# Kernel tuning notes

Measured on AMD Instinct MI355X. Metric: run time of the kernel, lower is better.

Reference implementation:

```python
import jax, jax.numpy as jnp
import numpy as np

HEAD_SIZE = 64


def setup_inputs() -> dict:
    key = jax.random.key(0)
    ks = jax.random.split(key, 10)
    B, S, D, H, hs = 4, 2048, 768, 12, HEAD_SIZE
    F = 4 * D
    sd = lambda n: 1.0 / np.sqrt(n)
    return {
        "x": jax.random.normal(ks[0], (B, S, D), jnp.float32),
        "Wq": jax.random.normal(ks[1], (H, D, hs), jnp.float32) * sd(D),
        "Wk": jax.random.normal(ks[2], (H, D, hs), jnp.float32) * sd(D),
        "Wv": jax.random.normal(ks[3], (H, D, hs), jnp.float32) * sd(D),
        "Wo": jax.random.normal(ks[4], (D, D), jnp.float32) * sd(D),
        "bo": jnp.zeros((D,), jnp.float32),
        "W1": jax.random.normal(ks[5], (D, F), jnp.float32) * sd(D),
        "b1": jnp.zeros((F,), jnp.float32),
        "W2": jax.random.normal(ks[6], (F, D), jnp.float32) * sd(F),
        "b2": jnp.zeros((D,), jnp.float32),
    }


def reference(x, Wq, Wk, Wv, Wo, bo, W1, b1, W2, b2):
    B, S, D = x.shape
    hs = Wq.shape[-1]
    # per-head projections (no bias), vectorized over heads: [B,H,S,hs]
    q = jnp.einsum("bsd,hde->bhse", x, Wq)
    k = jnp.einsum("bsd,hde->bhse", x, Wk)
    v = jnp.einsum("bsd,hde->bhse", x, Wv)
    # causal attention scores [B,H,S,S], scaled by sqrt(head_size)
    scores = jnp.einsum("bhse,bhte->bhst", q, k) / jnp.sqrt(jnp.float32(hs))
    causal = jnp.tril(jnp.ones((S, S), dtype=bool))
    scores = jnp.where(causal, scores, -jnp.inf)
    attn = jax.nn.softmax(scores, axis=-1)
    z = jnp.einsum("bhst,bhte->bhse", attn, v)
    # concat heads along feature dim (head order preserved) -> [B,S,D]
    z = z.transpose(0, 2, 1, 3).reshape(B, S, D)
    # output projection + residual
    z = z @ Wo + bo + x
    # FFN + residual
    h = jax.nn.relu(z @ W1 + b1)
    return h @ W2 + b2 + z
```

## Files before the change

### kernel.cpp

```cpp
#include <hip/hip_runtime.h>


typedef __attribute__((ext_vector_type(4))) float f32x4;
typedef __attribute__((ext_vector_type(8))) short bf16x8;
typedef __attribute__((ext_vector_type(4))) unsigned short u16x4;

#define GLB_AS __attribute__((address_space(1)))
#define LDS_AS __attribute__((address_space(3)))

__device__ __forceinline__ unsigned short f2bf(float f) {
  unsigned int u = __float_as_uint(f);
  u = (u + 0x7FFFu + ((u >> 16) & 1u)) >> 16;
  return (unsigned short)u;
}

__device__ __forceinline__ void gload16(const void* g, void* l) {
  __builtin_amdgcn_global_load_lds((const GLB_AS unsigned int*)g,
                                   (LDS_AS unsigned int*)l, 16, 0, 0);
}

__device__ __forceinline__ int xcd_swz(int orig, int nwg) {
  int q = nwg >> 3, r = nwg & 7;
  int xcd = orig & 7, rest = orig >> 3;
  return (xcd < r ? xcd * (q + 1) : r * (q + 1) + (xcd - r) * q) + rest;
}

#define VMW4 asm volatile("s_waitcnt vmcnt(4)" ::: "memory")
#define VMW0 asm volatile("s_waitcnt vmcnt(0)" ::: "memory")

__global__ void castx(const float* __restrict__ in, unsigned short* __restrict__ out, int n) {
  int i = (blockIdx.x * 256 + threadIdx.x) * 4;
  if (i < n) {
    float4 f = *(const float4*)&in[i];
    u16x4 o;
    o[0] = f2bf(f.x); o[1] = f2bf(f.y); o[2] = f2bf(f.z); o[3] = f2bf(f.w);
    *(u16x4*)&out[i] = o;
  }
}

__global__ void tcast(const float* __restrict__ in, unsigned short* __restrict__ out,
                      int R, int C, float scale) {
  __shared__ float tile[32][33];
  const float* inb = in + (size_t)blockIdx.z * R * C;
  unsigned short* outb = out + (size_t)blockIdx.z * R * C;
  int bx = blockIdx.x * 32;
  int by = blockIdx.y * 32;
  int tx = threadIdx.x, ty = threadIdx.y;
  #pragma unroll
  for (int i = 0; i < 32; i += 8)
    tile[ty + i][tx] = inb[(size_t)(by + ty + i) * C + bx + tx];
  __syncthreads();
  #pragma unroll
  for (int i = 0; i < 32; i += 8)
    outb[(size_t)(bx + ty + i) * R + by + tx] = f2bf(tile[tx][ty + i] * scale);
}

__global__ void tcast3(const float* __restrict__ Wq, const float* __restrict__ Wk,
                       const float* __restrict__ Wv, unsigned short* __restrict__ out,
                       float qscale) {
  __shared__ float tile[32][33];
  const int R = 768, C = 64;
  int z = blockIdx.z, wsel = z / 12, head = z % 12;
  const float* in = (wsel == 0 ? Wq : wsel == 1 ? Wk : Wv) + (size_t)head * R * C;
  unsigned short* outb = out + (size_t)wsel * R * R + (size_t)head * R * C;
  float scale = wsel == 0 ? qscale : 1.0f;
  int bx = blockIdx.x * 32;
  int by = blockIdx.y * 32;
  int tx = threadIdx.x, ty = threadIdx.y;
  #pragma unroll
  for (int i = 0; i < 32; i += 8)
    tile[ty + i][tx] = in[(size_t)(by + ty + i) * C + bx + tx];
  __syncthreads();
  #pragma unroll
  for (int i = 0; i < 32; i += 8)
    outb[(size_t)(bx + ty + i) * R + by + tx] = f2bf(tile[tx][ty + i] * scale);
}

__global__ void vtrans(const unsigned short* __restrict__ v, unsigned short* __restrict__ vT) {
  __shared__ unsigned short tile[32][33];
  int bh = blockIdx.z, b = bh / 12, h = bh % 12;
  int s0 = blockIdx.x * 32, e0 = blockIdx.y * 32;
  int tx = threadIdx.x, ty = threadIdx.y;
  #pragma unroll
  for (int i = 0; i < 32; i += 8)
    tile[ty + i][tx] = v[(size_t)(b * 2048 + s0 + ty + i) * 768 + h * 64 + e0 + tx];
  __syncthreads();
  #pragma unroll
  for (int i = 0; i < 32; i += 8)
    vT[(size_t)((b * 12 + h) * 64 + e0 + ty + i) * 2048 + s0 + tx] = tile[tx][ty + i];
}

template <int EPI, int MAP>
__global__ void gemm_bf16(const unsigned short* __restrict__ A,
                          const unsigned short* __restrict__ Bt,
                          const float* __restrict__ bias,
                          const float* __restrict__ resid,
                          float* __restrict__ Cf,
                          unsigned short* __restrict__ Cb,
                          int M, int N, int K, int gy, size_t segN) {
  __shared__ unsigned short Alds[2][128 * 32];
  __shared__ unsigned short Blds[2][128 * 32];
  const int tid = threadIdx.x;
  const int lane = tid & 63;
  const int w = tid >> 6;
  const int wm = w & 1, wn = w >> 1;

  int bm, bn;
  if constexpr (MAP == 1) {
    const int xcd = blockIdx.x & 7, rest = blockIdx.x >> 3;
    const int bnper = gy >> 3;
    bm = (rest / bnper) * 128;
    bn = (xcd * bnper + rest % bnper) * 128;
  } else if constexpr (MAP == 2) {
    const int xcd = blockIdx.x & 7, rest = blockIdx.x >> 3;
    if (rest < 128) { bm = (rest >> 1) * 128; bn = (xcd * 2 + (rest & 1)) * 128; }
    else { int r2 = rest - 128; bm = (xcd * 8 + (r2 & 7)) * 128; bn = (16 + (r2 >> 3)) * 128; }
  } else {
    const int wg = xcd_swz(blockIdx.x, gridDim.x);
    const int gsz = 8 * gy;
    const int group = wg / gsz;
    const int rem = wg - group * gsz;
    bm = (group * 8 + (rem & 7)) * 128;
    bn = (rem >> 3) * 128;
  }

  f32x4 acc[4][4] = {};

  const int r0 = tid >> 2;
  const int c0 = (tid & 3) * 8;

  #pragma unroll
  for (int i = 0; i < 2; ++i) {
    int row = r0 + i * 64;
    gload16(&A[(size_t)(bm + row) * K + c0], &Alds[0][row * 32 + c0]);
    gload16(&Bt[(size_t)(bn + row) * K + c0], &Blds[0][row * 32 + c0]);
  }
  __syncthreads();

  int buf = 0;
  for (int k0 = 0; k0 < K; k0 += 32) {
    if (k0 + 32 < K) {
      #pragma unroll
      for (int i = 0; i < 2; ++i) {
        int row = r0 + i * 64;
        gload16(&A[(size_t)(bm + row) * K + k0 + 32 + c0], &Alds[buf ^ 1][row * 32 + c0]);
        gload16(&Bt[(size_t)(bn + row) * K + k0 + 32 + c0], &Blds[buf ^ 1][row * 32 + c0]);
      }
      VMW4;
    } else {
      VMW0;
    }
    __builtin_amdgcn_s_barrier();

    bf16x8 af[4], bf[4];
    #pragma unroll
    for (int m = 0; m < 4; ++m)
      af[m] = *(const bf16x8*)&Alds[buf][(wm * 64 + m * 16 + (lane & 15)) * 32 + (lane >> 4) * 8];
    #pragma unroll
    for (int n = 0; n < 4; ++n)
      bf[n] = *(const bf16x8*)&Blds[buf][(wn * 64 + n * 16 + (lane & 15)) * 32 + (lane >> 4) * 8];
    #pragma unroll
    for (int m = 0; m < 4; ++m)
      #pragma unroll
      for (int n = 0; n < 4; ++n)
        acc[m][n] = __builtin_amdgcn_mfma_f32_16x16x32_bf16(af[m], bf[n], acc[m][n], 0, 0, 0);

    __builtin_amdgcn_s_barrier();
    buf ^= 1;
  }

  const int crow0 = bm + wm * 64 + ((lane >> 4)) * 4;
  const int ccol0 = bn + wn * 64 + (lane & 15);
  const int seg = bn / 768;
  const int lcol0 = (bn % 768) + wn * 64 + (lane & 15);
  #pragma unroll
  for (int m = 0; m < 4; ++m) {
    #pragma unroll
    for (int n = 0; n < 4; ++n) {
      int col = ccol0 + n * 16;
      #pragma unroll
      for (int r = 0; r < 4; ++r) {
        int row = crow0 + m * 16 + r;
        float v = acc[m][n][r];
        if constexpr (EPI & 1) v += bias[col];
        if constexpr (EPI & 4) v += resid[(size_t)row * N + col];
        if constexpr (EPI & 2) v = fmaxf(v, 0.f);
        if constexpr (EPI & 8) Cf[(size_t)row * N + col] = v;
        if constexpr (EPI & 16) Cb[(size_t)row * N + col] = f2bf(v);
        if constexpr (EPI & 32)
          Cb[(size_t)seg * segN + (size_t)row * 768 + lcol0 + n * 16] = f2bf(v);
      }
    }
  }
}

__global__ void attn_fwd(const unsigned short* __restrict__ q,
                         const unsigned short* __restrict__ k,
                         const unsigned short* __restrict__ vT,
                         unsigned short* __restrict__ z) {
  __shared__ unsigned short Klds[2 * 2 * 64 * 32];
  __shared__ unsigned short Vlds[2 * 2 * 64 * 32];
  __shared__ unsigned short Plds[4 * 16 * 72];

  const int wgid = xcd_swz(blockIdx.x, gridDim.x);
  const int pi = wgid & 15;
  const int bh = wgid >> 4;
  const int b = bh / 12, h = bh % 12;
  const int tid = threadIdx.x, lane = tid & 63, w = tid >> 6;
  const int q16 = lane & 15;
  const int qt  = lane >> 4;
  const int rdc = ((qt ^ ((q16 >> 1) & 3)) * 8);

  const int srow = tid >> 2;
  const int sdc  = (tid & 3) * 8;
  const int sgc  = (((tid & 3) ^ ((srow >> 1) & 3)) * 8);
  const size_t kbase = (size_t)(b * 2048) * 768 + h * 64;
  const size_t vbase = (size_t)((b * 12 + h) * 64) * 2048;
  unsigned short* Pw = &Plds[w * 16 * 72];

  #pragma unroll 1
  for (int seg = 0; seg < 2; ++seg) {
    const int qb = seg == 0 ? pi : 31 - pi;
    const int q0 = qb * 64;
    const int nt = qb + 1;

    const int qrow = q0 + w * 16 + q16;
    const size_t qoff = (size_t)(b * 2048 + qrow) * 768 + h * 64 + qt * 8;
    bf16x8 qf0 = *(const bf16x8*)&q[qoff];
    bf16x8 qf1 = *(const bf16x8*)&q[qoff + 32];

    f32x4 accO[4] = {};
    float lrow = 0.f;

    #pragma unroll
    for (int i = 0; i < 2; ++i) {
      gload16(&k[kbase + (size_t)srow * 768 + i * 32 + sgc],
              &Klds[i * 2048 + srow * 32 + sdc]);
      gload16(&vT[vbase + (size_t)srow * 2048 + i * 32 + sgc],
              &Vlds[i * 2048 + srow * 32 + sdc]);
    }
    __syncthreads();

    int buf = 0;
    for (int t = 0; t < nt; ++t) {
      if (t + 1 < nt) {
        const int kv1 = (t + 1) * 64;
        const int bo = (buf ^ 1) * 4096;
        #pragma unroll
        for (int i = 0; i < 2; ++i) {
          gload16(&k[kbase + (size_t)(kv1 + srow) * 768 + i * 32 + sgc],
                  &Klds[bo + i * 2048 + srow * 32 + sdc]);
          gload16(&vT[vbase + (size_t)srow * 2048 + kv1 + i * 32 + sgc],
                  &Vlds[bo + i * 2048 + srow * 32 + sdc]);
        }
        VMW4;
      } else {
        VMW0;
      }
      __builtin_amdgcn_s_barrier();

      const int kv0 = t * 64;
      const int kb_ = buf * 4096;

      bf16x8 kf0[4], kf1[4];
      #pragma unroll
      for (int n = 0; n < 4; ++n) {
        kf0[n] = *(const bf16x8*)&Klds[kb_ + 0 * 2048 + (n * 16 + q16) * 32 + rdc];
        kf1[n] = *(const bf16x8*)&Klds[kb_ + 1 * 2048 + (n * 16 + q16) * 32 + rdc];
      }
      f32x4 s[4];
      __builtin_amdgcn_s_setprio(1);
      #pragma unroll
      for (int n = 0; n < 4; ++n) {
        f32x4 zz = {};
        s[n] = __builtin_amdgcn_mfma_f32_16x16x32_bf16(kf0[n], qf0, zz, 0, 0, 0);
      }
      #pragma unroll
      for (int n = 0; n < 4; ++n)
        s[n] = __builtin_amdgcn_mfma_f32_16x16x32_bf16(kf1[n], qf1, s[n], 0, 0, 0);
      __builtin_amdgcn_s_setprio(0);

      if (t == nt - 1) {
        const int rowg = q0 + w * 16 + q16;
        #pragma unroll
        for (int n = 0; n < 4; ++n)
          #pragma unroll
          for (int r = 0; r < 4; ++r)
            if (kv0 + n * 16 + qt * 4 + r > rowg) s[n][r] = -3.0e38f;
      }

      #pragma unroll
      for (int n = 0; n < 4; ++n)
        #pragma unroll
        for (int r = 0; r < 4; ++r) { s[n][r] = exp2f(s[n][r]); lrow += s[n][r]; }

      #pragma unroll
      for (int n = 0; n < 4; ++n) {
        unsigned int lo, hi;
        asm("v_cvt_pk_bf16_f32 %0, %1, %2" : "=v"(lo) : "v"(s[n][0]), "v"(s[n][1]));
        asm("v_cvt_pk_bf16_f32 %0, %1, %2" : "=v"(hi) : "v"(s[n][2]), "v"(s[n][3]));
        uint2 pk; pk.x = lo; pk.y = hi;
        *(uint2*)&Pw[q16 * 72 + n * 16 + qt * 4] = pk;
      }

      __builtin_amdgcn_s_setprio(1);
      #pragma unroll
      for (int kk = 0; kk < 2; ++kk) {
        bf16x8 pf = *(const bf16x8*)&Pw[q16 * 72 + kk * 32 + qt * 8];
        #pragma unroll
        for (int n = 0; n < 4; ++n) {
          bf16x8 vf = *(const bf16x8*)&Vlds[kb_ + kk * 2048 + (n * 16 + q16) * 32 + rdc];
          accO[n] = __builtin_amdgcn_mfma_f32_16x16x32_bf16(pf, vf, accO[n], 0, 0, 0);
        }
      }
      __builtin_amdgcn_s_setprio(0);

      __builtin_amdgcn_s_barrier();
      buf ^= 1;
    }

    lrow += __shfl_xor(lrow, 16);
    lrow += __shfl_xor(lrow, 32);
    #pragma unroll
    for (int r = 0; r < 4; ++r) {
      float lr = __int_as_float(__builtin_amdgcn_ds_bpermute((qt * 4 + r) * 4,
                                                             __float_as_int(lrow)));
      float linv = 1.0f / lr;
      int rowg = q0 + w * 16 + qt * 4 + r;
      #pragma unroll
      for (int n = 0; n < 4; ++n)
        z[(size_t)(b * 2048 + rowg) * 768 + h * 64 + n * 16 + q16]
            = f2bf(accO[n][r] * linv);
    }
  }
}

extern "C" void kernel_launch(void* const* d_in, const int* in_sizes, int n_in,
                              void* d_out, int out_size, void* d_ws, size_t ws_size,
                              hipStream_t stream) {
  const float* x  = (const float*)d_in[0];
  const float* Wq = (const float*)d_in[1];
  const float* Wk = (const float*)d_in[2];
  const float* Wv = (const float*)d_in[3];
  const float* Wo = (const float*)d_in[4];
  const float* bo = (const float*)d_in[5];
  const float* W1 = (const float*)d_in[6];
  const float* b1 = (const float*)d_in[7];
  const float* W2 = (const float*)d_in[8];
  const float* b2 = (const float*)d_in[9];
  float* out = (float*)d_out;

  const int B = 4, S = 2048, D = 768, H = 12, hs = 64, F = 3072;
  const int M = B * S;
  const size_t MD = (size_t)M * D;

  unsigned short* xb   = (unsigned short*)d_ws;
  unsigned short* qb   = xb + MD;
  unsigned short* kb   = qb + MD;
  unsigned short* vb   = kb + MD;
  unsigned short* hbuf = xb;
  unsigned short* vT   = vb + MD;
  unsigned short* zb   = vT + MD;
  float*          z2f  = (float*)(zb + MD);
  unsigned short* z2b  = (unsigned short*)(z2f + MD);
  unsigned short* wqkvT= z2b + MD;
  unsigned short* woT  = wqkvT + 3 * (size_t)D * D;
  unsigned short* w1T  = woT + (size_t)D * D;
  unsigned short* w2T  = w1T + (size_t)D * F;

  dim3 tb(32, 8);

  castx<<<dim3((int)(MD / 4 / 256)), 256, 0, stream>>>(x, xb, (int)MD);

  const float QS = 0.125f * 1.4426950408889634f;
  tcast3<<<dim3(hs / 32, D / 32, 3 * H), tb, 0, stream>>>(Wq, Wk, Wv, wqkvT, QS);
  tcast<<<dim3(D / 32, D / 32, 1), tb, 0, stream>>>(Wo, woT, D, D, 1.0f);
  tcast<<<dim3(F / 32, D / 32, 1), tb, 0, stream>>>(W1, w1T, D, F, 1.0f);
  tcast<<<dim3(D / 32, F / 32, 1), tb, 0, stream>>>(W2, w2T, F, D, 1.0f);

  {
    int gy = 3 * D / 128;
    gemm_bf16<32, 2><<<dim3(64 * gy), 256, 0, stream>>>(xb, wqkvT, nullptr, nullptr,
                                                        nullptr, qb, M, 3 * D, D, gy, MD);
  }

  vtrans<<<dim3(S / 32, hs / 32, B * H), tb, 0, stream>>>(vb, vT);

  attn_fwd<<<dim3((S / 128) * B * H), 256, 0, stream>>>(qb, kb, vT, zb);

  {
    int gy = D / 128;
    gemm_bf16<1 | 4 | 8 | 16, 0><<<dim3(64 * gy), 256, 0, stream>>>(zb, woT, bo, x,
                                                                    z2f, z2b, M, D, D, gy, 0);
  }
  {
    int gy = F / 128;
    gemm_bf16<1 | 2 | 16, 1><<<dim3(64 * gy), 256, 0, stream>>>(z2b, w1T, b1, nullptr,
                                                                nullptr, hbuf, M, F, D, gy, 0);
  }
  {
    int gy = D / 128;
    gemm_bf16<1 | 4 | 8, 0><<<dim3(64 * gy), 256, 0, stream>>>(hbuf, w2T, b2, z2f,
                                                               out, nullptr, M, D, F, gy, 0);
  }
}
```

Before: 276.1 us.

## Fuse V transpose into QKV GEMM, merge weight casts, swizzle GEMM LDS

The QKV GEMM epilogue now writes the V head slice directly in transposed [b,h,e,s] layout, which removes the separate vtrans kernel and its extra pass over V. The three weight transpose-cast launches are merged into one tcastW launch to cut launch overhead. The GEMM LDS tile uses an XOR swizzle on the global source column and the fragment read column, meant to reduce LDS bank conflicts. The FFN1 GEMM switches from the XCD-column mapping to the default grouped mapping. The transposed V stores are strided along s, so the epilogue writes for that segment coalesce poorly.

Result: slower. 292.3 us (+5.9%).

```diff
diff --git a/kernel.cpp b/kernel.cpp
--- a/kernel.cpp
+++ b/kernel.cpp
@@ -36,23 +36,6 @@
     o[0] = f2bf(f.x); o[1] = f2bf(f.y); o[2] = f2bf(f.z); o[3] = f2bf(f.w);
     *(u16x4*)&out[i] = o;
   }
-}
-
-__global__ void tcast(const float* __restrict__ in, unsigned short* __restrict__ out,
-                      int R, int C, float scale) {
-  __shared__ float tile[32][33];
-  const float* inb = in + (size_t)blockIdx.z * R * C;
-  unsigned short* outb = out + (size_t)blockIdx.z * R * C;
-  int bx = blockIdx.x * 32;
-  int by = blockIdx.y * 32;
-  int tx = threadIdx.x, ty = threadIdx.y;
-  #pragma unroll
-  for (int i = 0; i < 32; i += 8)
-    tile[ty + i][tx] = inb[(size_t)(by + ty + i) * C + bx + tx];
-  __syncthreads();
-  #pragma unroll
-  for (int i = 0; i < 32; i += 8)
-    outb[(size_t)(bx + ty + i) * R + by + tx] = f2bf(tile[tx][ty + i] * scale);
 }
 
 __global__ void tcast3(const float* __restrict__ Wq, const float* __restrict__ Wk,
@@ -76,18 +59,26 @@
     outb[(size_t)(bx + ty + i) * R + by + tx] = f2bf(tile[tx][ty + i] * scale);
 }
 
-__global__ void vtrans(const unsigned short* __restrict__ v, unsigned short* __restrict__ vT) {
-  __shared__ unsigned short tile[32][33];
-  int bh = blockIdx.z, b = bh / 12, h = bh % 12;
-  int s0 = blockIdx.x * 32, e0 = blockIdx.y * 32;
+__global__ void tcastW(const float* __restrict__ Wo, const float* __restrict__ W1,
+                       const float* __restrict__ W2, unsigned short* __restrict__ woT,
+                       unsigned short* __restrict__ w1T, unsigned short* __restrict__ w2T) {
+  __shared__ float tile[32][33];
+  int id = blockIdx.x;
+  const float* in; unsigned short* out; int C, gx;
+  if (id < 576)       {           in = Wo; out = woT; C = 768;  gx = 24; }
+  else if (id < 2880) { id -= 576;  in = W1; out = w1T; C = 3072; gx = 96; }
+  else                { id -= 2880; in = W2; out = w2T; C = 768;  gx = 24; }
+  int bx = (id % gx) * 32;
+  int by = (id / gx) * 32;
   int tx = threadIdx.x, ty = threadIdx.y;
   #pragma unroll
   for (int i = 0; i < 32; i += 8)
-    tile[ty + i][tx] = v[(size_t)(b * 2048 + s0 + ty + i) * 768 + h * 64 + e0 + tx];
+    tile[ty + i][tx] = in[(size_t)(by + ty + i) * C + bx + tx];
   __syncthreads();
+  int R = (C == 768 && gx == 24 && in == W2) ? 3072 : 768;
   #pragma unroll
   for (int i = 0; i < 32; i += 8)
-    vT[(size_t)((b * 12 + h) * 64 + e0 + ty + i) * 2048 + s0 + tx] = tile[tx][ty + i];
+    out[(size_t)(bx + ty + i) * R + by + tx] = f2bf(tile[tx][ty + i]);
 }
 
 template <int EPI, int MAP>
@@ -97,6 +88,7 @@
                           const float* __restrict__ resid,
                           float* __restrict__ Cf,
                           unsigned short* __restrict__ Cb,
+                          unsigned short* __restrict__ Vt,
                           int M, int N, int K, int gy, size_t segN) {
   __shared__ unsigned short Alds[2][128 * 32];
   __shared__ unsigned short Blds[2][128 * 32];
@@ -106,12 +98,7 @@
   const int wm = w & 1, wn = w >> 1;
 
   int bm, bn;
-  if constexpr (MAP == 1) {
-    const int xcd = blockIdx.x & 7, rest = blockIdx.x >> 3;
-    const int bnper = gy >> 3;
-    bm = (rest / bnper) * 128;
-    bn = (xcd * bnper + rest % bnper) * 128;
-  } else if constexpr (MAP == 2) {
+  if constexpr (MAP == 2) {
     const int xcd = blockIdx.x & 7, rest = blockIdx.x >> 3;
     if (rest < 128) { bm = (rest >> 1) * 128; bn = (xcd * 2 + (rest & 1)) * 128; }
     else { int r2 = rest - 128; bm = (xcd * 8 + (r2 & 7)) * 128; bn = (16 + (r2 >> 3)) * 128; }
@@ -128,12 +115,14 @@
 
   const int r0 = tid >> 2;
   const int c0 = (tid & 3) * 8;
+  const int sg8 = ((tid & 3) ^ ((r0 >> 1) & 3)) * 8;
+  const int rc8 = (((lane >> 4)) ^ ((lane >> 1) & 3)) * 8;
 
   #pragma unroll
   for (int i = 0; i < 2; ++i) {
     int row = r0 + i * 64;
-    gload16(&A[(size_t)(bm + row) * K + c0], &Alds[0][row * 32 + c0]);
-    gload16(&Bt[(size_t)(bn + row) * K + c0], &Blds[0][row * 32 + c0]);
+    gload16(&A[(size_t)(bm + row) * K + sg8], &Alds[0][row * 32 + c0]);
+    gload16(&Bt[(size_t)(bn + row) * K + sg8], &Blds[0][row * 32 + c0]);
   }
   __syncthreads();
 
@@ -143,8 +132,8 @@
       #pragma unroll
       for (int i = 0; i < 2; ++i) {
         int row = r0 + i * 64;
-        gload16(&A[(size_t)(bm + row) * K + k0 + 32 + c0], &Alds[buf ^ 1][row * 32 + c0]);
-        gload16(&Bt[(size_t)(bn + row) * K + k0 + 32 + c0], &Blds[buf ^ 1][row * 32 + c0]);
+        gload16(&A[(size_t)(bm + row) * K + k0 + 32 + sg8], &Alds[buf ^ 1][row * 32 + c0]);
+        gload16(&Bt[(size_t)(bn + row) * K + k0 + 32 + sg8], &Blds[buf ^ 1][row * 32 + c0]);
       }
       VMW4;
     } else {
@@ -155,10 +144,10 @@
     bf16x8 af[4], bf[4];
     #pragma unroll
     for (int m = 0; m < 4; ++m)
-      af[m] = *(const bf16x8*)&Alds[buf][(wm * 64 + m * 16 + (lane & 15)) * 32 + (lane >> 4) * 8];
+      af[m] = *(const bf16x8*)&Alds[buf][(wm * 64 + m * 16 + (lane & 15)) * 32 + rc8];
     #pragma unroll
     for (int n = 0; n < 4; ++n)
-      bf[n] = *(const bf16x8*)&Blds[buf][(wn * 64 + n * 16 + (lane & 15)) * 32 + (lane >> 4) * 8];
+      bf[n] = *(const bf16x8*)&Blds[buf][(wn * 64 + n * 16 + (lane & 15)) * 32 + rc8];
     #pragma unroll
     for (int m = 0; m < 4; ++m)
       #pragma unroll
@@ -187,8 +176,16 @@
         if constexpr (EPI & 2) v = fmaxf(v, 0.f);
         if constexpr (EPI & 8) Cf[(size_t)row * N + col] = v;
         if constexpr (EPI & 16) Cb[(size_t)row * N + col] = f2bf(v);
-        if constexpr (EPI & 32)
-          Cb[(size_t)seg * segN + (size_t)row * 768 + lcol0 + n * 16] = f2bf(v);
+        if constexpr (EPI & 32) {
+          int lc = lcol0 + n * 16;
+          if ((EPI & 64) && seg == 2) {
+            int hh = lc >> 6, e = lc & 63;
+            int bb = row >> 11, s = row & 2047;
+            Vt[((size_t)(bb * 12 + hh) * 64 + e) * 2048 + s] = f2bf(v);
+          } else {
+            Cb[(size_t)seg * segN + (size_t)row * 768 + lc] = f2bf(v);
+          }
+        }
       }
     }
   }
@@ -374,33 +371,29 @@
 
   const float QS = 0.125f * 1.4426950408889634f;
   tcast3<<<dim3(hs / 32, D / 32, 3 * H), tb, 0, stream>>>(Wq, Wk, Wv, wqkvT, QS);
-  tcast<<<dim3(D / 32, D / 32, 1), tb, 0, stream>>>(Wo, woT, D, D, 1.0f);
-  tcast<<<dim3(F / 32, D / 32, 1), tb, 0, stream>>>(W1, w1T, D, F, 1.0f);
-  tcast<<<dim3(D / 32, F / 32, 1), tb, 0, stream>>>(W2, w2T, F, D, 1.0f);
+  tcastW<<<dim3(5184), tb, 0, stream>>>(Wo, W1, W2, woT, w1T, w2T);
 
   {
     int gy = 3 * D / 128;
-    gemm_bf16<32, 2><<<dim3(64 * gy), 256, 0, stream>>>(xb, wqkvT, nullptr, nullptr,
-                                                        nullptr, qb, M, 3 * D, D, gy, MD);
-  }
-
-  vtrans<<<dim3(S / 32, hs / 32, B * H), tb, 0, stream>>>(vb, vT);
+    gemm_bf16<32 | 64, 2><<<dim3(64 * gy), 256, 0, stream>>>(
+        xb, wqkvT, nullptr, nullptr, nullptr, qb, vT, M, 3 * D, D, gy, MD);
+  }
 
   attn_fwd<<<dim3((S / 128) * B * H), 256, 0, stream>>>(qb, kb, vT, zb);
 
   {
     int gy = D / 128;
-    gemm_bf16<1 | 4 | 8 | 16, 0><<<dim3(64 * gy), 256, 0, stream>>>(zb, woT, bo, x,
-                                                                    z2f, z2b, M, D, D, gy, 0);
+    gemm_bf16<1 | 4 | 8 | 16, 0><<<dim3(64 * gy), 256, 0, stream>>>(
+        zb, woT, bo, x, z2f, z2b, nullptr, M, D, D, gy, 0);
   }
   {
     int gy = F / 128;
-    gemm_bf16<1 | 2 | 16, 1><<<dim3(64 * gy), 256, 0, stream>>>(z2b, w1T, b1, nullptr,
-                                                                nullptr, hbuf, M, F, D, gy, 0);
+    gemm_bf16<1 | 2 | 16, 0><<<dim3(64 * gy), 256, 0, stream>>>(
+        z2b, w1T, b1, nullptr, nullptr, hbuf, nullptr, M, F, D, gy, 0);
   }
   {
     int gy = D / 128;
-    gemm_bf16<1 | 4 | 8, 0><<<dim3(64 * gy), 256, 0, stream>>>(hbuf, w2T, b2, z2f,
-                                                               out, nullptr, M, D, F, gy, 0);
-  }
-}
+    gemm_bf16<1 | 4 | 8, 0><<<dim3(64 * gy), 256, 0, stream>>>(
+        hbuf, w2T, b2, z2f, out, nullptr, nullptr, M, D, F, gy, 0);
+  }
+}
```
